# Optimization experiments

Measured on AMD Instinct MI355X. Metric: run time of the kernel, lower is better.

## Reference

```python
import jax, jax.numpy as jnp
import numpy as np

N_NODES = 50000
N_EDGES = 800000
N_GRAPHS = 64
IN_DIM = 128
HID4 = 256  # hidden_dim * 4
OUT_DIM = 256
EPS = 1e-5


def setup_inputs() -> dict:
    key = jax.random.key(0)
    ks = jax.random.split(key, 11)
    x = jax.random.normal(ks[0], (N_NODES, IN_DIM), jnp.float32)
    w = jax.random.uniform(ks[1], (N_EDGES,), jnp.float32)
    src = jax.random.randint(ks[2], (N_EDGES,), 0, N_NODES, dtype=jnp.int32)
    dst = jax.random.randint(ks[3], (N_EDGES,), 0, N_NODES, dtype=jnp.int32)
    graph_ids = jnp.sort(jax.random.randint(ks[4], (N_NODES,), 0, N_GRAPHS, dtype=jnp.int32))
    W1 = jax.random.normal(ks[5], (IN_DIM, HID4), jnp.float32) * 0.05
    Wfc = jax.random.normal(ks[6], (IN_DIM, HID4), jnp.float32) * 0.05
    gamma = jnp.ones((HID4,), jnp.float32)
    beta = jnp.zeros((HID4,), jnp.float32)
    W2 = jax.random.normal(ks[7], (2 * HID4, HID4), jnp.float32) * 0.05
    W3 = jax.random.normal(ks[8], (HID4, OUT_DIM), jnp.float32) * 0.05
    return {"x": x, "w": w, "W1": W1, "Wfc": Wfc, "gamma": gamma, "beta": beta,
            "W2": W2, "W3": W3, "src": src, "dst": dst, "graph_ids": graph_ids}


def _agg(h, src, dst, w, n):
    # edge-weighted SpMM: sum_{e: dst(e)=v} w_e * h[src(e)]
    return jax.ops.segment_sum(h[src] * w[:, None], dst, num_segments=n)


def _graph_conv(h, W, src, dst, w, out_norm, in_norm, n):
    # DGL GraphConv, norm='both', no bias, with edge_weight.
    h = h * out_norm  # D_out^{-1/2} on source side
    din, dout = W.shape
    if din > dout:  # DGL applies W first when it shrinks the width
        h = _agg(h @ W, src, dst, w, n)
    else:
        h = _agg(h, src, dst, w, n) @ W
    return h * in_norm  # D_in^{-1/2} on destination side


def _layer_norm(h, gamma, beta):
    mu = jnp.mean(h, axis=-1, keepdims=True)
    var = jnp.var(h, axis=-1, keepdims=True)
    return (h - mu) * jax.lax.rsqrt(var + EPS) * gamma + beta


def reference(x, w, W1, Wfc, gamma, beta, W2, W3, src, dst, graph_ids):
    n = x.shape[0]
    ones_e = jnp.ones(src.shape[0], jnp.float32)
    out_deg = jnp.maximum(jax.ops.segment_sum(ones_e, src, num_segments=n), 1.0)
    in_deg = jnp.maximum(jax.ops.segment_sum(ones_e, dst, num_segments=n), 1.0)
    out_norm = (out_deg ** -0.5)[:, None]
    in_norm = (in_deg ** -0.5)[:, None]

    x1 = jax.nn.relu(_graph_conv(x, W1, src, dst, w, out_norm, in_norm, n))
    f1 = jax.nn.relu(_layer_norm(x @ Wfc, gamma, beta))
    x1f1 = jnp.concatenate((x1, f1), axis=1)  # [N, 512]
    x2 = jax.nn.relu(_graph_conv(x1f1, W2, src, dst, w, out_norm, in_norm, n))
    x3 = jax.nn.relu(_graph_conv(x2, W3, src, dst, w, out_norm, in_norm, n))
    # dgl.sum_nodes: per-graph segment-sum readout
    readout = jax.ops.segment_sum(x3, graph_ids, num_segments=N_GRAPHS)
    return readout
```

## Files before the change

### kernel.cpp

```cpp
#include <hip/hip_runtime.h>

#define NN 50000
#define NE 800000
#define NG 64
#define EPSF 1e-5f

typedef __bf16 bf16x8 __attribute__((ext_vector_type(8)));
typedef float f32x4 __attribute__((ext_vector_type(4)));

#define AS1 __attribute__((address_space(1)))
#define AS3 __attribute__((address_space(3)))

__device__ __forceinline__ void gl_lds16(const unsigned short* g, unsigned short* l) {
#if __has_builtin(__builtin_amdgcn_global_load_lds)
  __builtin_amdgcn_global_load_lds((const AS1 void*)g, (AS3 void*)l, 16, 0, 0);
#else
  *(uint4*)l = *(const uint4*)g;
#endif
}

__device__ __forceinline__ unsigned short f2bf(float f) {
  unsigned u = __builtin_bit_cast(unsigned, f);
  u += 0x7fff + ((u >> 16) & 1);
  return (unsigned short)(u >> 16);
}
__device__ __forceinline__ float bf_lo(unsigned u) {
  return __builtin_bit_cast(float, u << 16);
}
__device__ __forceinline__ float bf_hi(unsigned u) {
  return __builtin_bit_cast(float, u & 0xffff0000u);
}

#define NB_H 128
#define EC   6250
#define RBINS 25000
#define RWORDS 12500
#define XB   1563
#define XTOT 1600000
#define WTB  256
__global__ __launch_bounds__(1024) void prep_kernel(
    const int* __restrict__ src, const int* __restrict__ dst,
    unsigned short* __restrict__ hout, unsigned short* __restrict__ hin,
    int* __restrict__ rank,
    const float* __restrict__ x, unsigned short* __restrict__ xb,
    const float* __restrict__ W1, const float* __restrict__ Wfc,
    const float* __restrict__ W2, const float* __restrict__ W3,
    unsigned short* __restrict__ W1t, unsigned short* __restrict__ Wfct,
    unsigned short* __restrict__ W2t, unsigned short* __restrict__ W3t) {
  __shared__ unsigned hist[RWORDS];
  int b = blockIdx.x;
  int tid = threadIdx.x;
  if (b < NB_H) {
    int e0 = b * EC;
#pragma unroll
    for (int ph = 0; ph < 2; ph++) {
      const int* key = ph ? src : dst;
      unsigned short* gh = (ph ? hout : hin) + (size_t)b * NN;
      for (int r = 0; r < 2; r++) {
        int lo = r * RBINS;
        for (int i = tid; i < RWORDS; i += 1024) hist[i] = 0u;
        __syncthreads();
        for (int i = tid; i < EC; i += 1024) {
          int k = key[e0 + i] - lo;
          if ((unsigned)k < (unsigned)RBINS) {
            int sh = (k & 1) << 4;
            unsigned old = atomicAdd(&hist[k >> 1], 1u << sh);
            if (ph == 0) rank[e0 + i] = (int)((old >> sh) & 0xffffu);
          }
        }
        __syncthreads();
        unsigned* gw = (unsigned*)(gh + lo);
        for (int i = tid; i < RWORDS; i += 1024) gw[i] = hist[i];
      }
    }
  } else if (b < NB_H + XB) {
    int i = (b - NB_H) * 1024 + tid;
    if (i < XTOT) {
      float4 v = ((const float4*)x)[i];
      uint2 pk;
      pk.x = (unsigned)f2bf(v.x) | ((unsigned)f2bf(v.y) << 16);
      pk.y = (unsigned)f2bf(v.z) | ((unsigned)f2bf(v.w) << 16);
      ((uint2*)xb)[i] = pk;
    }
  } else {
    int i = (b - NB_H - XB) * 1024 + tid;
    const float* W; unsigned short* Wt; int K, local;
    if (i < 32768)       { W = W1;  Wt = W1t;  K = 128; local = i; }
    else if (i < 65536)  { W = Wfc; Wt = Wfct; K = 128; local = i - 32768; }
    else if (i < 196608) { W = W2;  Wt = W2t;  K = 512; local = i - 65536; }
    else                 { W = W3;  Wt = W3t;  K = 256; local = i - 196608; }
    int n = local / K, k = local - n * K;
    Wt[local] = f2bf(W[(size_t)k * 256 + n]);
  }
}

__global__ void norms_scan1(const unsigned short* __restrict__ hout,
                            unsigned short* __restrict__ hin,
                            int* __restrict__ din,
                            float* __restrict__ onorm, float* __restrict__ inorm,
                            int* __restrict__ bsum, int n) {
  int i = blockIdx.x * 256 + threadIdx.x;
  int d = 0;
  if (i < n) {
    int a = 0;
    for (int b = 0; b < NB_H; b++) a += hout[(size_t)b * NN + i];
    int run = 0;
    for (int b = 0; b < NB_H; b++) {
      int t = hin[(size_t)b * NN + i];
      hin[(size_t)b * NN + i] = (unsigned short)run;
      run += t;
    }
    d = run;
    din[i] = run;
    onorm[i] = rsqrtf((float)(a > 1 ? a : 1));
    inorm[i] = rsqrtf((float)(d > 1 ? d : 1));
  }
  int v = d;
#pragma unroll
  for (int off = 32; off > 0; off >>= 1) v += __shfl_down(v, off);
  __shared__ int ws[4];
  int wave = threadIdx.x >> 6, lane = threadIdx.x & 63;
  if (lane == 0) ws[wave] = v;
  __syncthreads();
  if (threadIdx.x == 0) bsum[blockIdx.x] = ws[0] + ws[1] + ws[2] + ws[3];
}

__global__ void scan3_kernel(const int* __restrict__ din, const int* __restrict__ bsum,
                             int* __restrict__ rp, int n, int nb) {
  int t = threadIdx.x;
  int lane = t & 63, wave = t >> 6;
  int bj = (t < nb) ? bsum[t] : 0;
  int pre = (t < (int)blockIdx.x) ? bj : 0;
  int p = pre, q = bj;
#pragma unroll
  for (int off = 32; off > 0; off >>= 1) {
    p += __shfl_down(p, off);
    q += __shfl_down(q, off);
  }
  __shared__ int red[8];
  __shared__ int baseS, totS;
  if (lane == 0) { red[wave] = p; red[4 + wave] = q; }
  __syncthreads();
  if (t == 0) {
    baseS = red[0] + red[1] + red[2] + red[3];
    totS  = red[4] + red[5] + red[6] + red[7];
  }
  __syncthreads();
  int i = blockIdx.x * 256 + t;
  int v = (i < n) ? din[i] : 0;
  __shared__ int tmp[256];
  tmp[t] = v;
  __syncthreads();
  for (int off = 1; off < 256; off <<= 1) {
    int x = (t >= off) ? tmp[t - off] : 0;
    __syncthreads();
    tmp[t] += x;
    __syncthreads();
  }
  if (i < n) rp[i] = tmp[t] - v + baseS;
  if (blockIdx.x == gridDim.x - 1 && t == 0) rp[n] = totS;
}

__global__ void fill_kernel(const int* __restrict__ src, const int* __restrict__ dst,
                            const float* __restrict__ w, const float* __restrict__ onorm,
                            const float* __restrict__ inorm,
                            const int* __restrict__ rp, const int* __restrict__ rank,
                            const unsigned short* __restrict__ binBase,
                            int* __restrict__ col, float* __restrict__ wse, int E) {
  int e = blockIdx.x * 256 + threadIdx.x;
  if (e < E) {
    int d = dst[e], s = src[e];
    int b = e / EC;
    int pos = rp[d] + (int)binBase[(size_t)b * NN + d] + rank[e];
    col[pos] = s;
    wse[pos] = w[e] * onorm[s] * inorm[d];
  }
}

template <int RELU, int NU>
__global__ __launch_bounds__(64) void spmm_bf16(
    const unsigned short* __restrict__ feat, int ldf,
    const int* __restrict__ rp, const int* __restrict__ col,
    const float* __restrict__ wse,
    unsigned short* __restrict__ out, int ldo) {
  int v = blockIdx.x;
  int t = threadIdx.x;
  int beg = rp[v], end = rp[v + 1];
  float acc[2 * NU];
#pragma unroll
  for (int i = 0; i < 2 * NU; i++) acc[i] = 0.f;
  const unsigned short* base = feat + t * (2 * NU);
  int e = beg;
  for (; e + 8 <= end; e += 8) {
    int s[8]; float ww[8];
#pragma unroll
    for (int k = 0; k < 8; k++) { s[k] = col[e + k]; ww[k] = wse[e + k]; }
    unsigned u[8][NU];
#pragma unroll
    for (int k = 0; k < 8; k++) {
      const unsigned* pr = (const unsigned*)&base[(size_t)s[k] * ldf];
      if (NU == 2) { uint2 q = *(const uint2*)pr; u[k][0] = q.x; u[k][NU - 1] = q.y; }
      else u[k][0] = pr[0];
    }
#pragma unroll
    for (int k = 0; k < 8; k++)
#pragma unroll
      for (int j = 0; j < NU; j++) {
        acc[2 * j]     += ww[k] * bf_lo(u[k][j]);
        acc[2 * j + 1] += ww[k] * bf_hi(u[k][j]);
      }
  }
  for (; e < end; e++) {
    float w0 = wse[e];
    const unsigned* pr = (const unsigned*)&base[(size_t)col[e] * ldf];
    unsigned u[NU];
    if (NU == 2) { uint2 q = *(const uint2*)pr; u[0] = q.x; u[NU - 1] = q.y; }
    else u[0] = pr[0];
#pragma unroll
    for (int j = 0; j < NU; j++) {
      acc[2 * j]     += w0 * bf_lo(u[j]);
      acc[2 * j + 1] += w0 * bf_hi(u[j]);
    }
  }
  unsigned o[NU];
#pragma unroll
  for (int j = 0; j < NU; j++) {
    float a = acc[2 * j], b = acc[2 * j + 1];
    if (RELU) { a = fmaxf(a, 0.f); b = fmaxf(b, 0.f); }
    o[j] = (unsigned)f2bf(a) | ((unsigned)f2bf(b) << 16);
  }
  unsigned* po = (unsigned*)&out[(size_t)v * ldo + t * (2 * NU)];
  if (NU == 2) *(uint2*)po = make_uint2(o[0], o[NU - 1]);
  else po[0] = o[0];
}

__device__ __forceinline__ void gemm_body(
    const unsigned short* __restrict__ A, int lda,
    const unsigned short* __restrict__ Bt, int K,
    unsigned short* __restrict__ C, int ldc, int col_off, int M,
    int relu,
    unsigned short* As, unsigned short* Bs) {
  const int tid = threadIdx.x;
  const int lane = tid & 63;
  const int w = tid >> 6;
  const int wm = w >> 1, wn = w & 1;
  const int m0 = blockIdx.x * 128;
  const int n0 = blockIdx.y * 128;
  const int q = lane >> 4;
  const int r16 = lane & 15;

  f32x4 acc[4][4];
#pragma unroll
  for (int i = 0; i < 4; i++)
#pragma unroll
    for (int j = 0; j < 4; j++) acc[i][j] = (f32x4){0.f, 0.f, 0.f, 0.f};

  const int ta = 2 * w, tb = 2 * w + 1;
  int gma = m0 + ta * 16 + r16; if (gma >= M) gma = M - 1;
  int gmb = m0 + tb * 16 + r16; if (gmb >= M) gmb = M - 1;
  const int gna = n0 + ta * 16 + r16;
  const int gnb = n0 + tb * 16 + r16;
  const unsigned short* pa = A + (size_t)gma * lda + q * 8;
  const unsigned short* pb = A + (size_t)gmb * lda + q * 8;
  const unsigned short* pc = Bt + (size_t)gna * K + q * 8;
  const unsigned short* pd = Bt + (size_t)gnb * K + q * 8;

  for (int k0 = 0; k0 < K; k0 += 32) {
    __syncthreads();
    gl_lds16(pa + k0, &As[ta * 512 + lane * 8]);
    gl_lds16(pb + k0, &As[tb * 512 + lane * 8]);
    gl_lds16(pc + k0, &Bs[ta * 512 + lane * 8]);
    gl_lds16(pd + k0, &Bs[tb * 512 + lane * 8]);
    __syncthreads();

    bf16x8 af[4], bfr[4];
#pragma unroll
    for (int i = 0; i < 4; i++)
      af[i] = *(const bf16x8*)&As[(wm * 4 + i) * 512 + lane * 8];
#pragma unroll
    for (int j = 0; j < 4; j++)
      bfr[j] = *(const bf16x8*)&Bs[(wn * 4 + j) * 512 + lane * 8];
#pragma unroll
    for (int i = 0; i < 4; i++)
#pragma unroll
      for (int j = 0; j < 4; j++)
        acc[i][j] = __builtin_amdgcn_mfma_f32_16x16x32_bf16(af[i], bfr[j], acc[i][j], 0, 0, 0);
  }

#pragma unroll
  for (int i = 0; i < 4; i++) {
    int rbase = m0 + (wm * 4 + i) * 16 + q * 4;
#pragma unroll
    for (int r = 0; r < 4; r++) {
      int gm = rbase + r;
      if (gm >= M) continue;
#pragma unroll
      for (int j = 0; j < 4; j++) {
        float v = acc[i][j][r];
        if (relu) v = fmaxf(v, 0.f);
        int gn = col_off + n0 + (wn * 4 + j) * 16 + r16;
        C[(size_t)gm * ldc + gn] = f2bf(v);
      }
    }
  }
}

__global__ __launch_bounds__(256) void gemm12_kernel(
    const unsigned short* __restrict__ A0, const unsigned short* __restrict__ B0,
    const unsigned short* __restrict__ A1, const unsigned short* __restrict__ B1,
    unsigned short* __restrict__ C, int M) {
  __shared__ unsigned short As[8 * 512];
  __shared__ unsigned short Bs[8 * 512];
  int z = blockIdx.z;
  gemm_body(z ? A1 : A0, 128, z ? B1 : B0, 128, C, 512, z * 256, M, z == 0, As, Bs);
}

__global__ __launch_bounds__(256) void gemm_kernel(
    const unsigned short* __restrict__ A, int lda,
    const unsigned short* __restrict__ Bt, int K,
    unsigned short* __restrict__ C, int ldc, int M, int relu) {
  __shared__ unsigned short As[8 * 512];
  __shared__ unsigned short Bs[8 * 512];
  gemm_body(A, lda, Bt, K, C, ldc, 0, M, relu, As, Bs);
}

__global__ void ln_relu_bf16(unsigned short* __restrict__ h, int ld,
                             const float* __restrict__ gamma,
                             const float* __restrict__ beta) {
  int v = blockIdx.x;
  int f = threadIdx.x;
  float val = bf_lo((unsigned)h[(size_t)v * ld + f]);
  float s = val, qq = val * val;
#pragma unroll
  for (int off = 32; off > 0; off >>= 1) {
    s += __shfl_down(s, off);
    qq += __shfl_down(qq, off);
  }
  __shared__ float ws_[5], wq_[5];
  int wave = f >> 6, lane = f & 63;
  if (lane == 0) { ws_[wave] = s; wq_[wave] = qq; }
  __syncthreads();
  if (f == 0) {
    float S = 0, Q = 0;
    for (int i = 0; i < 4; i++) { S += ws_[i]; Q += wq_[i]; }
    ws_[4] = S; wq_[4] = Q;
  }
  __syncthreads();
  float mean = ws_[4] * (1.f / 256.f);
  float var = wq_[4] * (1.f / 256.f) - mean * mean;
  float y = (val - mean) * rsqrtf(var + EPSF) * gamma[f] + beta[f];
  h[(size_t)v * ld + f] = f2bf(y > 0.f ? y : 0.f);
}

__global__ void readout_kernel(const unsigned short* __restrict__ x3,
                               const int* __restrict__ gid,
                               float* __restrict__ out, int n) {
  int g = blockIdx.x;
  int part = blockIdx.y;
  int f = threadIdx.x;
  int lo = 0, hi = n;
  while (lo < hi) { int mid = (lo + hi) >> 1; if (gid[mid] < g) lo = mid + 1; else hi = mid; }
  int s = lo;
  lo = s; hi = n;
  while (lo < hi) { int mid = (lo + hi) >> 1; if (gid[mid] < g + 1) lo = mid + 1; else hi = mid; }
  int e = lo;
  int len = e - s;
  if (len <= 0) return;
  int chunk = (len + 7) / 8;
  int cs = s + part * chunk;
  int ce = cs + chunk; if (ce > e) ce = e;
  if (cs >= ce) return;
  float acc = 0.f;
  for (int v = cs; v < ce; v++) acc += bf_lo((unsigned)x3[(size_t)v * 256 + f]);
  atomicAdd(&out[g * 256 + f], acc);
}


extern "C" void kernel_launch(void* const* d_in, const int* in_sizes, int n_in,
                              void* d_out, int out_size, void* d_ws, size_t ws_size,
                              hipStream_t stream) {
  const float* x     = (const float*)d_in[0];
  const float* w     = (const float*)d_in[1];
  const float* W1    = (const float*)d_in[2];
  const float* Wfc   = (const float*)d_in[3];
  const float* gamma = (const float*)d_in[4];
  const float* beta  = (const float*)d_in[5];
  const float* W2    = (const float*)d_in[6];
  const float* W3    = (const float*)d_in[7];
  const int*   src   = (const int*)d_in[8];
  const int*   dst   = (const int*)d_in[9];
  const int*   gid   = (const int*)d_in[10];
  float* out = (float*)d_out;

  const int N = NN, E = NE;

  char* p = (char*)d_ws;
  auto alloc = [&](size_t bytes) {
    char* r = p;
    p += (bytes + 255) & ~(size_t)255;
    return r;
  };
  unsigned short* hout = (unsigned short*)alloc((size_t)NB_H * N * 2);
  unsigned short* hin  = (unsigned short*)alloc((size_t)NB_H * N * 2);
  int*   din     = (int*)alloc((size_t)N * 4);
  float* onorm   = (float*)alloc((size_t)N * 4);
  float* inorm   = (float*)alloc((size_t)N * 4);
  int*   row_ptr = (int*)alloc((size_t)(N + 1) * 4);
  int*   bsum    = (int*)alloc(256 * 4);
  int*   rank    = (int*)alloc((size_t)E * 4);
  int*   col     = (int*)alloc((size_t)E * 4);
  float* wse     = (float*)alloc((size_t)E * 4);
  unsigned short* xb    = (unsigned short*)alloc((size_t)N * 128 * 2);
  unsigned short* aggX  = (unsigned short*)alloc((size_t)N * 128 * 2);
  unsigned short* x1f1  = (unsigned short*)alloc((size_t)N * 512 * 2);
  unsigned short* y2    = (unsigned short*)alloc((size_t)N * 256 * 2);
  unsigned short* x2    = (unsigned short*)alloc((size_t)N * 256 * 2);
  unsigned short* aggx2 = (unsigned short*)alloc((size_t)N * 256 * 2);
  unsigned short* W1t   = (unsigned short*)alloc((size_t)256 * 128 * 2);
  unsigned short* Wfct  = (unsigned short*)alloc((size_t)256 * 128 * 2);
  unsigned short* W2t   = (unsigned short*)alloc((size_t)256 * 512 * 2);
  unsigned short* W3t   = (unsigned short*)alloc((size_t)256 * 256 * 2);
  unsigned short* x3 = x1f1;

  hipMemsetAsync(out, 0, (size_t)NG * 256 * 4, stream);

  const int nbS = (N + 255) / 256;

  prep_kernel<<<NB_H + XB + WTB, 1024, 0, stream>>>(src, dst, hout, hin, rank,
                                                    x, xb, W1, Wfc, W2, W3,
                                                    W1t, Wfct, W2t, W3t);
  norms_scan1<<<nbS, 256, 0, stream>>>(hout, hin, din, onorm, inorm, bsum, N);
  scan3_kernel<<<nbS, 256, 0, stream>>>(din, bsum, row_ptr, N, nbS);
  fill_kernel<<<(E + 255) / 256, 256, 0, stream>>>(src, dst, w, onorm, inorm, row_ptr,
                                                   rank, hin, col, wse, E);

  dim3 ggrid((N + 127) / 128, 2);
  dim3 ggridz((N + 127) / 128, 2, 2);

  spmm_bf16<0, 1><<<N, 64, 0, stream>>>(xb, 128, row_ptr, col, wse, aggX, 128);
  gemm12_kernel<<<ggridz, 256, 0, stream>>>(aggX, W1t, xb, Wfct, x1f1, N);
  ln_relu_bf16<<<N, 256, 0, stream>>>(x1f1 + 256, 512, gamma, beta);
  gemm_kernel<<<ggrid, 256, 0, stream>>>(x1f1, 512, W2t, 512, y2, 256, N, 0);
  spmm_bf16<1, 2><<<N, 64, 0, stream>>>(y2, 256, row_ptr, col, wse, x2, 256);
  spmm_bf16<0, 2><<<N, 64, 0, stream>>>(x2, 256, row_ptr, col, wse, aggx2, 256);
  gemm_kernel<<<ggrid, 256, 0, stream>>>(aggx2, 256, W3t, 256, x3, 256, N, 1);
  readout_kernel<<<dim3(NG, 8), 256, 0, stream>>>(x3, gid, out, N);
}
```

Measured before the change: 471.8 us.

## Pack edge arrays, use byte-wide histograms, widen GEMM tile to full N

Three separate changes. The CSR column index and weight arrays become one interleaved uint2 edge array, so SpMM fetches each edge with a single 8-byte load. The degree histograms in the prep kernel drop from 16-bit to 8-bit packed counters, which lets one pass cover all bins over larger edge chunks; this relies on no per-chunk bin count exceeding 255. The GEMM now computes all 256 output columns per block, so each A tile is loaded once instead of twice, at the cost of doubling the accumulators and B shared memory, which may lower occupancy.

```diff
diff --git a/kernel.cpp b/kernel.cpp
--- a/kernel.cpp
+++ b/kernel.cpp
@@ -31,23 +31,22 @@
   return __builtin_bit_cast(float, u & 0xffff0000u);
 }
 
-#define NB_H 128
-#define EC   6250
-#define RBINS 25000
-#define RWORDS 12500
+#define NB_H 64
+#define EC   12500
+#define HWORDS 12500
 #define XB   1563
 #define XTOT 1600000
 #define WTB  256
 __global__ __launch_bounds__(1024) void prep_kernel(
     const int* __restrict__ src, const int* __restrict__ dst,
-    unsigned short* __restrict__ hout, unsigned short* __restrict__ hin,
+    unsigned char* __restrict__ hout, unsigned char* __restrict__ hin,
     int* __restrict__ rank,
     const float* __restrict__ x, unsigned short* __restrict__ xb,
     const float* __restrict__ W1, const float* __restrict__ Wfc,
     const float* __restrict__ W2, const float* __restrict__ W3,
     unsigned short* __restrict__ W1t, unsigned short* __restrict__ Wfct,
     unsigned short* __restrict__ W2t, unsigned short* __restrict__ W3t) {
-  __shared__ unsigned hist[RWORDS];
+  __shared__ unsigned hist[HWORDS];
   int b = blockIdx.x;
   int tid = threadIdx.x;
   if (b < NB_H) {
@@ -55,23 +54,19 @@
 #pragma unroll
     for (int ph = 0; ph < 2; ph++) {
       const int* key = ph ? src : dst;
-      unsigned short* gh = (ph ? hout : hin) + (size_t)b * NN;
-      for (int r = 0; r < 2; r++) {
-        int lo = r * RBINS;
-        for (int i = tid; i < RWORDS; i += 1024) hist[i] = 0u;
-        __syncthreads();
-        for (int i = tid; i < EC; i += 1024) {
-          int k = key[e0 + i] - lo;
-          if ((unsigned)k < (unsigned)RBINS) {
-            int sh = (k & 1) << 4;
-            unsigned old = atomicAdd(&hist[k >> 1], 1u << sh);
-            if (ph == 0) rank[e0 + i] = (int)((old >> sh) & 0xffffu);
-          }
-        }
-        __syncthreads();
-        unsigned* gw = (unsigned*)(gh + lo);
-        for (int i = tid; i < RWORDS; i += 1024) gw[i] = hist[i];
+      unsigned char* gh = (ph ? hout : hin) + (size_t)b * NN;
+      for (int i = tid; i < HWORDS; i += 1024) hist[i] = 0u;
+      __syncthreads();
+      for (int i = tid; i < EC; i += 1024) {
+        int k = key[e0 + i];
+        int sh = (k & 3) << 3;
+        unsigned old = atomicAdd(&hist[k >> 2], 1u << sh);
+        if (ph == 0) rank[e0 + i] = (int)((old >> sh) & 0xffu);
       }
+      __syncthreads();
+      unsigned* gw = (unsigned*)gh;
+      for (int i = tid; i < HWORDS; i += 1024) gw[i] = hist[i];
+      __syncthreads();
     }
   } else if (b < NB_H + XB) {
     int i = (b - NB_H) * 1024 + tid;
@@ -94,8 +89,8 @@
   }
 }
 
-__global__ void norms_scan1(const unsigned short* __restrict__ hout,
-                            unsigned short* __restrict__ hin,
+__global__ void norms_scan1(const unsigned char* __restrict__ hout,
+                            unsigned char* __restrict__ hin,
                             int* __restrict__ din,
                             float* __restrict__ onorm, float* __restrict__ inorm,
                             int* __restrict__ bsum, int n) {
@@ -107,7 +102,7 @@
     int run = 0;
     for (int b = 0; b < NB_H; b++) {
       int t = hin[(size_t)b * NN + i];
-      hin[(size_t)b * NN + i] = (unsigned short)run;
+      hin[(size_t)b * NN + i] = (unsigned char)run;
       run += t;
     }
     d = run;
@@ -165,23 +160,22 @@
                             const float* __restrict__ w, const float* __restrict__ onorm,
                             const float* __restrict__ inorm,
                             const int* __restrict__ rp, const int* __restrict__ rank,
-                            const unsigned short* __restrict__ binBase,
-                            int* __restrict__ col, float* __restrict__ wse, int E) {
+                            const unsigned char* __restrict__ binBase,
+                            uint2* __restrict__ edge, int E) {
   int e = blockIdx.x * 256 + threadIdx.x;
   if (e < E) {
     int d = dst[e], s = src[e];
     int b = e / EC;
     int pos = rp[d] + (int)binBase[(size_t)b * NN + d] + rank[e];
-    col[pos] = s;
-    wse[pos] = w[e] * onorm[s] * inorm[d];
+    float wv = w[e] * onorm[s] * inorm[d];
+    edge[pos] = make_uint2((unsigned)s, __builtin_bit_cast(unsigned, wv));
   }
 }
 
 template <int RELU, int NU>
 __global__ __launch_bounds__(64) void spmm_bf16(
     const unsigned short* __restrict__ feat, int ldf,
-    const int* __restrict__ rp, const int* __restrict__ col,
-    const float* __restrict__ wse,
+    const int* __restrict__ rp, const uint2* __restrict__ edge,
     unsigned short* __restrict__ out, int ldo) {
   int v = blockIdx.x;
   int t = threadIdx.x;
@@ -194,7 +188,11 @@
   for (; e + 8 <= end; e += 8) {
     int s[8]; float ww[8];
 #pragma unroll
-    for (int k = 0; k < 8; k++) { s[k] = col[e + k]; ww[k] = wse[e + k]; }
+    for (int k = 0; k < 8; k++) {
+      uint2 q = edge[e + k];
+      s[k] = (int)q.x;
+      ww[k] = __builtin_bit_cast(float, q.y);
+    }
     unsigned u[8][NU];
 #pragma unroll
     for (int k = 0; k < 8; k++) {
@@ -211,8 +209,9 @@
       }
   }
   for (; e < end; e++) {
-    float w0 = wse[e];
-    const unsigned* pr = (const unsigned*)&base[(size_t)col[e] * ldf];
+    uint2 qe = edge[e];
+    float w0 = __builtin_bit_cast(float, qe.y);
+    const unsigned* pr = (const unsigned*)&base[(size_t)qe.x * ldf];
     unsigned u[NU];
     if (NU == 2) { uint2 q = *(const uint2*)pr; u[0] = q.x; u[NU - 1] = q.y; }
     else u[0] = pr[0];
@@ -234,62 +233,60 @@
   else po[0] = o[0];
 }
 
-__device__ __forceinline__ void gemm_body(
+__device__ __forceinline__ void gemm256_body(
     const unsigned short* __restrict__ A, int lda,
     const unsigned short* __restrict__ Bt, int K,
     unsigned short* __restrict__ C, int ldc, int col_off, int M,
-    int relu,
-    unsigned short* As, unsigned short* Bs) {
+    int relu, unsigned short* As, unsigned short* Bs) {
   const int tid = threadIdx.x;
   const int lane = tid & 63;
   const int w = tid >> 6;
-  const int wm = w >> 1, wn = w & 1;
-  const int m0 = blockIdx.x * 128;
-  const int n0 = blockIdx.y * 128;
   const int q = lane >> 4;
   const int r16 = lane & 15;
-
-  f32x4 acc[4][4];
-#pragma unroll
-  for (int i = 0; i < 4; i++)
+  const int m0 = blockIdx.x * 128;
+
+  f32x4 acc[8][4];
+#pragma unroll
+  for (int i = 0; i < 8; i++)
 #pragma unroll
     for (int j = 0; j < 4; j++) acc[i][j] = (f32x4){0.f, 0.f, 0.f, 0.f};
 
-  const int ta = 2 * w, tb = 2 * w + 1;
-  int gma = m0 + ta * 16 + r16; if (gma >= M) gma = M - 1;
-  int gmb = m0 + tb * 16 + r16; if (gmb >= M) gmb = M - 1;
-  const int gna = n0 + ta * 16 + r16;
-  const int gnb = n0 + tb * 16 + r16;
-  const unsigned short* pa = A + (size_t)gma * lda + q * 8;
-  const unsigned short* pb = A + (size_t)gmb * lda + q * 8;
-  const unsigned short* pc = Bt + (size_t)gna * K + q * 8;
-  const unsigned short* pd = Bt + (size_t)gnb * K + q * 8;
+  int ga0 = m0 + (2 * w) * 16 + r16;     if (ga0 >= M) ga0 = M - 1;
+  int ga1 = m0 + (2 * w + 1) * 16 + r16; if (ga1 >= M) ga1 = M - 1;
+  const unsigned short* pa0 = A + (size_t)ga0 * lda + q * 8;
+  const unsigned short* pa1 = A + (size_t)ga1 * lda + q * 8;
+  const unsigned short* pbt[4];
+#pragma unroll
+  for (int t = 0; t < 4; t++) {
+    int gn = (4 * w + t) * 16 + r16;
+    pbt[t] = Bt + (size_t)gn * K + q * 8;
+  }
 
   for (int k0 = 0; k0 < K; k0 += 32) {
     __syncthreads();
-    gl_lds16(pa + k0, &As[ta * 512 + lane * 8]);
-    gl_lds16(pb + k0, &As[tb * 512 + lane * 8]);
-    gl_lds16(pc + k0, &Bs[ta * 512 + lane * 8]);
-    gl_lds16(pd + k0, &Bs[tb * 512 + lane * 8]);
+    gl_lds16(pa0 + k0, &As[(2 * w) * 512 + lane * 8]);
+    gl_lds16(pa1 + k0, &As[(2 * w + 1) * 512 + lane * 8]);
+#pragma unroll
+    for (int t = 0; t < 4; t++)
+      gl_lds16(pbt[t] + k0, &Bs[(4 * w + t) * 512 + lane * 8]);
     __syncthreads();
 
-    bf16x8 af[4], bfr[4];
-#pragma unroll
-    for (int i = 0; i < 4; i++)
-      af[i] = *(const bf16x8*)&As[(wm * 4 + i) * 512 + lane * 8];
+    bf16x8 bfr[4];
 #pragma unroll
     for (int j = 0; j < 4; j++)
-      bfr[j] = *(const bf16x8*)&Bs[(wn * 4 + j) * 512 + lane * 8];
-#pragma unroll
-    for (int i = 0; i < 4; i++)
+      bfr[j] = *(const bf16x8*)&Bs[(4 * w + j) * 512 + lane * 8];
+#pragma unroll
+    for (int i = 0; i < 8; i++) {
+      bf16x8 af = *(const bf16x8*)&As[i * 512 + lane * 8];
 #pragma unroll
       for (int j = 0; j < 4; j++)
-        acc[i][j] = __builtin_amdgcn_mfma_f32_16x16x32_bf16(af[i], bfr[j], acc[i][j], 0, 0, 0);
-  }
-
-#pragma unroll
-  for (int i = 0; i < 4; i++) {
-    int rbase = m0 + (wm * 4 + i) * 16 + q * 4;
+        acc[i][j] = __builtin_amdgcn_mfma_f32_16x16x32_bf16(af, bfr[j], acc[i][j], 0, 0, 0);
+    }
+  }
+
+#pragma unroll
+  for (int i = 0; i < 8; i++) {
+    int rbase = m0 + i * 16 + q * 4;
 #pragma unroll
     for (int r = 0; r < 4; r++) {
       int gm = rbase + r;
@@ -298,7 +295,7 @@
       for (int j = 0; j < 4; j++) {
         float v = acc[i][j][r];
         if (relu) v = fmaxf(v, 0.f);
-        int gn = col_off + n0 + (wn * 4 + j) * 16 + r16;
+        int gn = col_off + (4 * w + j) * 16 + r16;
         C[(size_t)gm * ldc + gn] = f2bf(v);
       }
     }
@@ -310,9 +307,9 @@
     const unsigned short* __restrict__ A1, const unsigned short* __restrict__ B1,
     unsigned short* __restrict__ C, int M) {
   __shared__ unsigned short As[8 * 512];
-  __shared__ unsigned short Bs[8 * 512];
+  __shared__ unsigned short Bs[16 * 512];
   int z = blockIdx.z;
-  gemm_body(z ? A1 : A0, 128, z ? B1 : B0, 128, C, 512, z * 256, M, z == 0, As, Bs);
+  gemm256_body(z ? A1 : A0, 128, z ? B1 : B0, 128, C, 512, z * 256, M, z == 0, As, Bs);
 }
 
 __global__ __launch_bounds__(256) void gemm_kernel(
@@ -320,8 +317,8 @@
     const unsigned short* __restrict__ Bt, int K,
     unsigned short* __restrict__ C, int ldc, int M, int relu) {
   __shared__ unsigned short As[8 * 512];
-  __shared__ unsigned short Bs[8 * 512];
-  gemm_body(A, lda, Bt, K, C, ldc, 0, M, relu, As, Bs);
+  __shared__ unsigned short Bs[16 * 512];
+  gemm256_body(A, lda, Bt, K, C, ldc, 0, M, relu, As, Bs);
 }
 
 __global__ void ln_relu_bf16(unsigned short* __restrict__ h, int ld,
@@ -400,16 +397,15 @@
     p += (bytes + 255) & ~(size_t)255;
     return r;
   };
-  unsigned short* hout = (unsigned short*)alloc((size_t)NB_H * N * 2);
-  unsigned short* hin  = (unsigned short*)alloc((size_t)NB_H * N * 2);
+  unsigned char* hout = (unsigned char*)alloc((size_t)NB_H * N);
+  unsigned char* hin  = (unsigned char*)alloc((size_t)NB_H * N);
   int*   din     = (int*)alloc((size_t)N * 4);
   float* onorm   = (float*)alloc((size_t)N * 4);
   float* inorm   = (float*)alloc((size_t)N * 4);
   int*   row_ptr = (int*)alloc((size_t)(N + 1) * 4);
   int*   bsum    = (int*)alloc(256 * 4);
   int*   rank    = (int*)alloc((size_t)E * 4);
-  int*   col     = (int*)alloc((size_t)E * 4);
-  float* wse     = (float*)alloc((size_t)E * 4);
+  uint2* edge    = (uint2*)alloc((size_t)E * 8);
   unsigned short* xb    = (unsigned short*)alloc((size_t)N * 128 * 2);
   unsigned short* aggX  = (unsigned short*)alloc((size_t)N * 128 * 2);
   unsigned short* x1f1  = (unsigned short*)alloc((size_t)N * 512 * 2);
@@ -432,17 +428,17 @@
   norms_scan1<<<nbS, 256, 0, stream>>>(hout, hin, din, onorm, inorm, bsum, N);
   scan3_kernel<<<nbS, 256, 0, stream>>>(din, bsum, row_ptr, N, nbS);
   fill_kernel<<<(E + 255) / 256, 256, 0, stream>>>(src, dst, w, onorm, inorm, row_ptr,
-                                                   rank, hin, col, wse, E);
-
-  dim3 ggrid((N + 127) / 128, 2);
-  dim3 ggridz((N + 127) / 128, 2, 2);
-
-  spmm_bf16<0, 1><<<N, 64, 0, stream>>>(xb, 128, row_ptr, col, wse, aggX, 128);
+                                                   rank, hin, edge, E);
+
+  dim3 ggrid((N + 127) / 128, 1);
+  dim3 ggridz((N + 127) / 128, 1, 2);
+
+  spmm_bf16<0, 1><<<N, 64, 0, stream>>>(xb, 128, row_ptr, edge, aggX, 128);
   gemm12_kernel<<<ggridz, 256, 0, stream>>>(aggX, W1t, xb, Wfct, x1f1, N);
   ln_relu_bf16<<<N, 256, 0, stream>>>(x1f1 + 256, 512, gamma, beta);
   gemm_kernel<<<ggrid, 256, 0, stream>>>(x1f1, 512, W2t, 512, y2, 256, N, 0);
-  spmm_bf16<1, 2><<<N, 64, 0, stream>>>(y2, 256, row_ptr, col, wse, x2, 256);
-  spmm_bf16<0, 2><<<N, 64, 0, stream>>>(x2, 256, row_ptr, col, wse, aggx2, 256);
+  spmm_bf16<1, 2><<<N, 64, 0, stream>>>(y2, 256, row_ptr, edge, x2, 256);
+  spmm_bf16<0, 2><<<N, 64, 0, stream>>>(x2, 256, row_ptr, edge, aggx2, 256);
   gemm_kernel<<<ggrid, 256, 0, stream>>>(aggx2, 256, W3t, 256, x3, 256, N, 1);
   readout_kernel<<<dim3(NG, 8), 256, 0, stream>>>(x3, gid, out, N);
 }
```

After: 461.4 us. 1.02x faster.
